# Performance work log

Measured on AMD Instinct MI355X. Metric: run time of the kernel, lower is better.

## Reference

```python
import jax, jax.numpy as jnp
import numpy as np

N_NODES = 50000
N_EDGES = 300000
F_IN, HID, N_CLS = 256, 256, 128


def _glorot_linear(key, fan_in, fan_out):
    # torch.nn.Linear-style uniform init, kaiming bound 1/sqrt(fan_in)
    s = 1.0 / np.sqrt(fan_in)
    return jax.random.uniform(key, (fan_in, fan_out), jnp.float32, -s, s)


def setup_inputs() -> dict:
    key = jax.random.key(0)
    ks = jax.random.split(key, 8)
    x = jax.random.normal(ks[0], (N_NODES, F_IN), jnp.float32)
    edge_index = jax.random.randint(ks[1], (2, N_EDGES), 0, N_NODES, dtype=jnp.int32)
    return {
        "x": x,
        "edge_index": edge_index,
        "W1": _glorot_linear(ks[2], F_IN, HID), "b1": jnp.zeros((HID,), jnp.float32),
        "W2": _glorot_linear(ks[3], HID, HID),  "b2": jnp.zeros((HID,), jnp.float32),
        "W3": _glorot_linear(ks[4], HID, HID),  "b3": jnp.zeros((HID,), jnp.float32),
        "W4": _glorot_linear(ks[5], HID, N_CLS), "b4": jnp.zeros((N_CLS,), jnp.float32),
    }


def _gcn_conv(x, W, b, src, dst, norm, n):
    # x' = D^{-1/2} (A + I) D^{-1/2} X W + b   (PyG GCNConv default)
    h = x @ W                                  # [N, out]
    msg = h[src] * norm[:, None]               # gather + edge scaling  [E', out]
    return jax.ops.segment_sum(msg, dst, num_segments=n) + b


def reference(x, edge_index, W1, b1, W2, b2, W3, b3, W4, b4):
    n = x.shape[0]
    loops = jnp.arange(n, dtype=edge_index.dtype)
    src = jnp.concatenate([edge_index[0], loops])  # add self-loops
    dst = jnp.concatenate([edge_index[1], loops])
    # symmetric normalization: deg over target nodes (unit edge weights)
    deg = jax.ops.segment_sum(jnp.ones_like(dst, jnp.float32), dst, num_segments=n)
    dis = jnp.where(deg > 0, jax.lax.rsqrt(jnp.maximum(deg, 1.0)), 0.0)
    norm = dis[src] * dis[dst]                     # [E']

    h = jax.nn.relu(_gcn_conv(x, W1, b1, src, dst, norm, n))
    h = jax.nn.relu(_gcn_conv(h, W2, b2, src, dst, norm, n))
    h = jax.nn.relu(_gcn_conv(h, W3, b3, src, dst, norm, n))
    h = _gcn_conv(h, W4, b4, src, dst, norm, n)    # [N, C]

    # global_add_pool with batch == zeros -> single-graph sum pool
    pooled = jnp.sum(h, axis=0, keepdims=True)     # [1, C]
    return (pooled, jax.nn.log_softmax(pooled, axis=1))
```

## Files before the change

### kernel.cpp

```cpp
#include <hip/hip_runtime.h>


typedef __attribute__((ext_vector_type(8))) short short8;
typedef __attribute__((ext_vector_type(4))) float float4v;

__device__ __forceinline__ unsigned short f2b(float f) {
    unsigned int u = __builtin_bit_cast(unsigned int, f);
    u += 0x7fffu + ((u >> 16) & 1u);
    return (unsigned short)(u >> 16);
}
__device__ __forceinline__ float b2f(unsigned short b) {
    unsigned int u = ((unsigned int)b) << 16;
    return __builtin_bit_cast(float, u);
}


__global__ void zero_kernel(int* __restrict__ cnt, float* __restrict__ tsum,
                            float* __restrict__ acc, int N) {
    int i = blockIdx.x * 256 + threadIdx.x;
    if (i < N) { cnt[i] = 0; tsum[i] = 0.f; }
    if (i < 256) acc[i] = 0.f;
}

__global__ void count_kernel(const int* __restrict__ dst, int* __restrict__ cnt, int E) {
    int i = blockIdx.x * blockDim.x + threadIdx.x;
    if (i < E) atomicAdd(&cnt[dst[i]], 1);
}

__global__ void blocksum_kernel(const int* __restrict__ cnt, int* __restrict__ bsum, int N) {
    __shared__ int s[256];
    int t = threadIdx.x;
    int i = blockIdx.x * 256 + t;
    s[t] = (i < N) ? cnt[i] : 0;
    __syncthreads();
    for (int d = 128; d > 0; d >>= 1) {
        if (t < d) s[t] += s[t + d];
        __syncthreads();
    }
    if (t == 0) bsum[blockIdx.x] = s[0];
}

__global__ void finalize_kernel(const int* __restrict__ cnt, const int* __restrict__ bsum,
                                int* __restrict__ offs, int* __restrict__ cursor,
                                float* __restrict__ dis, int N, int E, int nb) {
    __shared__ int bs[256];
    __shared__ int s[256];
    int t = threadIdx.x;
    bs[t] = (t < nb) ? bsum[t] : 0;
    __syncthreads();
    for (int d = 1; d < 256; d <<= 1) {
        int x = (t >= d) ? bs[t - d] : 0;
        __syncthreads();
        bs[t] += x;
        __syncthreads();
    }
    int blockoff = (blockIdx.x == 0) ? 0 : bs[blockIdx.x - 1];
    int i = blockIdx.x * 256 + t;
    int c = (i < N) ? cnt[i] : 0;
    s[t] = c;
    __syncthreads();
    for (int d = 1; d < 256; d <<= 1) {
        int x = (t >= d) ? s[t - d] : 0;
        __syncthreads();
        s[t] += x;
        __syncthreads();
    }
    if (i < N) {
        int ex = blockoff + s[t] - c;
        offs[i] = ex;
        cursor[i] = ex;
        dis[i] = rsqrtf((float)(c + 1));
    }
    if (blockIdx.x == 0 && t == 0) offs[N] = E;
}

__global__ void scatter_outsum_kernel(const int* __restrict__ src, const int* __restrict__ dst,
                                      const float* __restrict__ dis, int* __restrict__ cursor,
                                      int* __restrict__ csr_src, float* __restrict__ csr_nrm,
                                      float* __restrict__ tsum, int E) {
    int i = blockIdx.x * blockDim.x + threadIdx.x;
    if (i < E) {
        int s = src[i], d = dst[i];
        float dd = dis[d];
        int pos = atomicAdd(&cursor[d], 1);
        csr_src[pos] = s;
        csr_nrm[pos] = dis[s] * dd;
        atomicAdd(&tsum[s], dd);
    }
}


__global__ void convert_wt_kernel(const float* __restrict__ W1, const float* __restrict__ W2,
                                  const float* __restrict__ W3, unsigned short* __restrict__ Wt1,
                                  unsigned short* __restrict__ Wt2, unsigned short* __restrict__ Wt3) {
    const float* W = (blockIdx.y == 0) ? W1 : (blockIdx.y == 1) ? W2 : W3;
    unsigned short* Wt = (blockIdx.y == 0) ? Wt1 : (blockIdx.y == 1) ? Wt2 : Wt3;
    int n = blockIdx.x;
    int k = threadIdx.x;
    Wt[n * 256 + k] = f2b(W[k * 256 + n]);
}

template <int AFP32>
__global__ __launch_bounds__(256, 3) void gemm_bf16_kernel(
        const void* __restrict__ Ap, const unsigned short* __restrict__ Wt,
        unsigned short* __restrict__ C, int M) {
    __shared__ unsigned short As[128 * 64];
    __shared__ unsigned short Bs[128 * 64];
    const int tid = threadIdx.x;
    const int lane = tid & 63;
    const int wave = tid >> 6;
    const int l15 = lane & 15;
    const int quad = lane >> 4;
    const int wm = wave & 1;
    const int wn = wave >> 1;
    const int m0 = blockIdx.x * 128;
    const int n0 = blockIdx.y * 128;

    float4v acc[4][4] = {};

    const int lrow = lane >> 3;
    const int lslot = (lane & 7) ^ lrow;

    const unsigned short* Bt = Wt + (size_t)n0 * 256;

    for (int kk = 0; kk < 256; kk += 64) {
        if (AFP32) {
            const float* Af = (const float*)Ap;
            const int srow = tid >> 3;
            const int slot = tid & 7;
#pragma unroll
            for (int p = 0; p < 4; p++) {
                int row = p * 32 + srow;
                int gm = m0 + row;
                float4 lo = make_float4(0.f, 0.f, 0.f, 0.f);
                float4 hi = make_float4(0.f, 0.f, 0.f, 0.f);
                if (gm < M) {
                    const float* ap = &Af[(size_t)gm * 256 + kk + slot * 8];
                    lo = *(const float4*)ap;
                    hi = *(const float4*)(ap + 4);
                }
                union { unsigned short u[8]; float4 v; } pk;
                pk.u[0] = f2b(lo.x); pk.u[1] = f2b(lo.y);
                pk.u[2] = f2b(lo.z); pk.u[3] = f2b(lo.w);
                pk.u[4] = f2b(hi.x); pk.u[5] = f2b(hi.y);
                pk.u[6] = f2b(hi.z); pk.u[7] = f2b(hi.w);
                *(float4*)&As[row * 64 + 8 * (slot ^ (row & 7))] = pk.v;
            }
        } else {
            const unsigned short* Ab = (const unsigned short*)Ap;
#pragma unroll
            for (int i = 0; i < 4; i++) {
                int r0 = wave * 32 + i * 8;
                int gm = m0 + r0 + lrow;
                if (gm >= M) gm = M - 1;
                const unsigned short* gp = &Ab[(size_t)gm * 256 + kk + lslot * 8];
                __builtin_amdgcn_global_load_lds(
                    (const __attribute__((address_space(1))) unsigned int*)gp,
                    (__attribute__((address_space(3))) unsigned int*)&As[r0 * 64],
                    16, 0, 0);
            }
        }
#pragma unroll
        for (int i = 0; i < 4; i++) {
            int r0 = wave * 32 + i * 8;
            const unsigned short* gp = &Bt[(size_t)(r0 + lrow) * 256 + kk + lslot * 8];
            __builtin_amdgcn_global_load_lds(
                (const __attribute__((address_space(1))) unsigned int*)gp,
                (__attribute__((address_space(3))) unsigned int*)&Bs[r0 * 64],
                16, 0, 0);
        }
        __syncthreads();
#pragma unroll
        for (int ks = 0; ks < 64; ks += 32) {
            const int sl = (ks >> 3) + quad;
            short8 af[4], bf[4];
#pragma unroll
            for (int mi = 0; mi < 4; mi++) {
                int row = wm * 64 + mi * 16 + l15;
                af[mi] = *(const short8*)&As[row * 64 + 8 * (sl ^ (row & 7))];
            }
#pragma unroll
            for (int nj = 0; nj < 4; nj++) {
                int row = wn * 64 + nj * 16 + l15;
                bf[nj] = *(const short8*)&Bs[row * 64 + 8 * (sl ^ (row & 7))];
            }
#pragma unroll
            for (int mi = 0; mi < 4; mi++)
#pragma unroll
                for (int nj = 0; nj < 4; nj++)
                    acc[mi][nj] = __builtin_amdgcn_mfma_f32_16x16x32_bf16(
                        af[mi], bf[nj], acc[mi][nj], 0, 0, 0);
        }
        __syncthreads();
    }

#pragma unroll
    for (int mi = 0; mi < 4; mi++) {
#pragma unroll
        for (int r = 0; r < 4; r++) {
            int row = m0 + wm * 64 + mi * 16 + quad * 4 + r;
            if (row < M) {
#pragma unroll
                for (int nj = 0; nj < 4; nj++) {
                    int col = n0 + wn * 64 + nj * 16 + l15;
                    C[(size_t)row * 256 + col] = f2b(acc[mi][nj][r]);
                }
            }
        }
    }
}

template <int RELU>
__global__ __launch_bounds__(256) void agg_bf16_kernel(
        const unsigned short* __restrict__ T, const float* __restrict__ bias,
        const int* __restrict__ offs, const int* __restrict__ csr_src,
        const float* __restrict__ csr_nrm, const float* __restrict__ dis,
        unsigned short* __restrict__ out, int N) {
    int hw = threadIdx.x >> 5;
    int l = threadIdx.x & 31;
    int v = blockIdx.x * 8 + hw;
    if (v >= N) return;
    int f8 = l * 8;
    int beg = offs[v], end = offs[v + 1];
    float dv = dis[v];
    float w = dv * dv;
    float a[8];
    {
        short8 hs = *(const short8*)&T[(size_t)v * 256 + f8];
#pragma unroll
        for (int i = 0; i < 8; i++) a[i] = w * b2f((unsigned short)hs[i]);
    }
    int e = beg;
    for (; e + 4 <= end; e += 4) {
        int s0 = csr_src[e],     s1 = csr_src[e + 1];
        int s2 = csr_src[e + 2], s3 = csr_src[e + 3];
        float n0 = csr_nrm[e],     n1 = csr_nrm[e + 1];
        float n2 = csr_nrm[e + 2], n3 = csr_nrm[e + 3];
        short8 h0 = *(const short8*)&T[(size_t)s0 * 256 + f8];
        short8 h1 = *(const short8*)&T[(size_t)s1 * 256 + f8];
        short8 h2 = *(const short8*)&T[(size_t)s2 * 256 + f8];
        short8 h3 = *(const short8*)&T[(size_t)s3 * 256 + f8];
#pragma unroll
        for (int i = 0; i < 8; i++)
            a[i] += n0 * b2f((unsigned short)h0[i]) + n1 * b2f((unsigned short)h1[i])
                  + n2 * b2f((unsigned short)h2[i]) + n3 * b2f((unsigned short)h3[i]);
    }
    for (; e < end; e++) {
        int s = csr_src[e];
        float nm = csr_nrm[e];
        short8 h = *(const short8*)&T[(size_t)s * 256 + f8];
#pragma unroll
        for (int i = 0; i < 8; i++) a[i] += nm * b2f((unsigned short)h[i]);
    }
    float4 bv0 = *(const float4*)&bias[f8];
    float4 bv1 = *(const float4*)&bias[f8 + 4];
    a[0] += bv0.x; a[1] += bv0.y; a[2] += bv0.z; a[3] += bv0.w;
    a[4] += bv1.x; a[5] += bv1.y; a[6] += bv1.z; a[7] += bv1.w;
    if (RELU) {
#pragma unroll
        for (int i = 0; i < 8; i++) a[i] = fmaxf(a[i], 0.f);
    }
    uint4 o;
    o.x = (unsigned int)f2b(a[0]) | ((unsigned int)f2b(a[1]) << 16);
    o.y = (unsigned int)f2b(a[2]) | ((unsigned int)f2b(a[3]) << 16);
    o.z = (unsigned int)f2b(a[4]) | ((unsigned int)f2b(a[5]) << 16);
    o.w = (unsigned int)f2b(a[6]) | ((unsigned int)f2b(a[7]) << 16);
    *(uint4*)&out[(size_t)v * 256 + f8] = o;
}

__global__ __launch_bounds__(256) void wpool_partial(
        const unsigned short* __restrict__ H, const float* __restrict__ dis,
        const float* __restrict__ tsum, float* __restrict__ partial, int N) {
    int tid = threadIdx.x;
    int f8 = (tid & 31) * 8;
    int rg = tid >> 5;
    float a[8] = {};
    for (int r = blockIdx.x * 8 + rg; r < N; r += gridDim.x * 8) {
        float s = dis[r] * (dis[r] + tsum[r]);
        short8 h = *(const short8*)&H[(size_t)r * 256 + f8];
#pragma unroll
        for (int i = 0; i < 8; i++) a[i] += s * b2f((unsigned short)h[i]);
    }
    __shared__ float red[8 * 256];
#pragma unroll
    for (int i = 0; i < 8; i++) red[rg * 256 + f8 + i] = a[i];
    __syncthreads();
    for (int s = 4; s > 0; s >>= 1) {
        if (rg < s) {
#pragma unroll
            for (int i = 0; i < 8; i++)
                red[rg * 256 + f8 + i] += red[(rg + s) * 256 + f8 + i];
        }
        __syncthreads();
    }
    partial[(size_t)blockIdx.x * 256 + tid] = red[tid];
}

__global__ void wpool_reduce(const float* __restrict__ partial, float* __restrict__ acc) {
    int f = threadIdx.x;
    int p0 = blockIdx.x * 32;
    float a = 0.f;
#pragma unroll
    for (int p = 0; p < 32; p++) a += partial[(size_t)(p0 + p) * 256 + f];
    atomicAdd(&acc[f], a);
}

__global__ void final_kernel(const float* __restrict__ acc, const float* __restrict__ W4,
                             const float* __restrict__ b4, float* __restrict__ out, int N) {
    __shared__ float red[128];
    int c = threadIdx.x;
    float p = (float)N * b4[c];
    for (int k = 0; k < 256; k++) p += acc[k] * W4[k * 128 + c];
    out[c] = p;
    red[c] = p;
    __syncthreads();
    for (int s = 64; s > 0; s >>= 1) {
        if (c < s) red[c] = fmaxf(red[c], red[c + s]);
        __syncthreads();
    }
    float m = red[0];
    __syncthreads();
    red[c] = expf(p - m);
    __syncthreads();
    for (int s = 64; s > 0; s >>= 1) {
        if (c < s) red[c] += red[c + s];
        __syncthreads();
    }
    float lse = m + logf(red[0]);
    out[128 + c] = p - lse;
}

extern "C" void kernel_launch(void* const* d_in, const int* in_sizes, int n_in,
                              void* d_out, int out_size, void* d_ws, size_t ws_size,
                              hipStream_t stream) {
    const float* x  = (const float*)d_in[0];
    const int*   ei = (const int*)d_in[1];
    const float* W1 = (const float*)d_in[2];
    const float* b1 = (const float*)d_in[3];
    const float* W2 = (const float*)d_in[4];
    const float* b2 = (const float*)d_in[5];
    const float* W3 = (const float*)d_in[6];
    const float* b3 = (const float*)d_in[7];
    const float* W4 = (const float*)d_in[8];
    const float* b4 = (const float*)d_in[9];

    const int N = in_sizes[0] / 256;
    const int E = in_sizes[1] / 2;
    const int* src = ei;
    const int* dst = ei + E;

    char* p = (char*)d_ws;
    auto alloc = [&](size_t bytes) {
        char* r = p;
        p += (bytes + 255) & ~(size_t)255;
        return r;
    };
    int*            cnt     = (int*)alloc((size_t)N * 4);
    int*            offs    = (int*)alloc((size_t)(N + 1) * 4);
    int*            cursor  = (int*)alloc((size_t)N * 4);
    float*          dis     = (float*)alloc((size_t)N * 4);
    float*          tsum    = (float*)alloc((size_t)N * 4);
    int*            bsum    = (int*)alloc(1024 * 4);
    int*            csr_src = (int*)alloc((size_t)E * 4);
    float*          csr_nrm = (float*)alloc((size_t)E * 4);
    unsigned short* Wt1     = (unsigned short*)alloc(256 * 256 * 2);
    unsigned short* Wt2     = (unsigned short*)alloc(256 * 256 * 2);
    unsigned short* Wt3     = (unsigned short*)alloc(256 * 256 * 2);
    unsigned short* T       = (unsigned short*)alloc((size_t)N * 256 * 2);
    unsigned short* Abuf    = (unsigned short*)alloc((size_t)N * 256 * 2);
    float*          partial = (float*)alloc((size_t)1024 * 256 * 4);
    float*          accbuf  = (float*)alloc(256 * 4);

    int eb = (E + 255) / 256;
    int nb = (N + 255) / 256;
    zero_kernel<<<nb, 256, 0, stream>>>(cnt, tsum, accbuf, N);
    count_kernel<<<eb, 256, 0, stream>>>(dst, cnt, E);
    blocksum_kernel<<<nb, 256, 0, stream>>>(cnt, bsum, N);
    finalize_kernel<<<nb, 256, 0, stream>>>(cnt, bsum, offs, cursor, dis, N, E, nb);
    scatter_outsum_kernel<<<eb, 256, 0, stream>>>(src, dst, dis, cursor, csr_src,
                                                  csr_nrm, tsum, E);

    convert_wt_kernel<<<dim3(256, 3), 256, 0, stream>>>(W1, W2, W3, Wt1, Wt2, Wt3);

    dim3 ggrid((N + 127) / 128, 2);
    int ab = (N + 7) / 8;
    gemm_bf16_kernel<1><<<ggrid, 256, 0, stream>>>(x, Wt1, T, N);
    agg_bf16_kernel<1><<<ab, 256, 0, stream>>>(T, b1, offs, csr_src, csr_nrm, dis, Abuf, N);
    gemm_bf16_kernel<0><<<ggrid, 256, 0, stream>>>(Abuf, Wt2, T, N);
    agg_bf16_kernel<1><<<ab, 256, 0, stream>>>(T, b2, offs, csr_src, csr_nrm, dis, Abuf, N);
    gemm_bf16_kernel<0><<<ggrid, 256, 0, stream>>>(Abuf, Wt3, T, N);
    agg_bf16_kernel<1><<<ab, 256, 0, stream>>>(T, b3, offs, csr_src, csr_nrm, dis, Abuf, N);

    wpool_partial<<<1024, 256, 0, stream>>>(Abuf, dis, tsum, partial, N);
    wpool_reduce<<<32, 256, 0, stream>>>(partial, accbuf);
    final_kernel<<<1, 128, 0, stream>>>(accbuf, W4, b4, (float*)d_out, N);
}
```

Baseline: 312.0 us.

## Degree-sort nodes for aggregation balance and merge small setup kernels

Builds a permutation of nodes bucketed by in-degree (histogram in finalize, counting-sort in a new kernel) so aggregation half-waves in a block process nodes of similar degree, reducing divergence and imbalance. Also fuses the zeroing and weight-conversion kernels into one launch. It drops the separate pool-reduce kernel by having the final kernel sum 256 partials directly. This adds an extra indirection per node, costs locality of output writes, and makes the final kernel do a serial reduction in a single block.

```diff
diff --git a/kernel.cpp b/kernel.cpp
--- a/kernel.cpp
+++ b/kernel.cpp
@@ -14,12 +14,26 @@
     return __builtin_bit_cast(float, u);
 }
 
-
-__global__ void zero_kernel(int* __restrict__ cnt, float* __restrict__ tsum,
-                            float* __restrict__ acc, int N) {
-    int i = blockIdx.x * 256 + threadIdx.x;
-    if (i < N) { cnt[i] = 0; tsum[i] = 0.f; }
-    if (i < 256) acc[i] = 0.f;
+__global__ void zero_convert_kernel(int* __restrict__ cnt, float* __restrict__ tsum,
+                                    int* __restrict__ hist, int* __restrict__ hcur,
+                                    const float* __restrict__ W1, const float* __restrict__ W2,
+                                    const float* __restrict__ W3, unsigned short* __restrict__ Wt1,
+                                    unsigned short* __restrict__ Wt2, unsigned short* __restrict__ Wt3,
+                                    int N, int nb) {
+    int t = threadIdx.x;
+    int b = blockIdx.x;
+    if (b < nb) {
+        int i = b * 256 + t;
+        if (i < N) { cnt[i] = 0; tsum[i] = 0.f; }
+        if (b == 0 && t < 64) { hist[t] = 0; hcur[t] = 0; }
+    } else {
+        int bb = b - nb;
+        int w = bb >> 8;
+        int n = bb & 255;
+        const float* W = (w == 0) ? W1 : (w == 1) ? W2 : W3;
+        unsigned short* Wt = (w == 0) ? Wt1 : (w == 1) ? Wt2 : Wt3;
+        Wt[n * 256 + t] = f2b(W[t * 256 + n]);
+    }
 }
 
 __global__ void count_kernel(const int* __restrict__ dst, int* __restrict__ cnt, int E) {
@@ -42,7 +56,8 @@
 
 __global__ void finalize_kernel(const int* __restrict__ cnt, const int* __restrict__ bsum,
                                 int* __restrict__ offs, int* __restrict__ cursor,
-                                float* __restrict__ dis, int N, int E, int nb) {
+                                float* __restrict__ dis, int* __restrict__ hist,
+                                int N, int E, int nb) {
     __shared__ int bs[256];
     __shared__ int s[256];
     int t = threadIdx.x;
@@ -70,6 +85,7 @@
         offs[i] = ex;
         cursor[i] = ex;
         dis[i] = rsqrtf((float)(c + 1));
+        atomicAdd(&hist[c < 63 ? c : 63], 1);
     }
     if (blockIdx.x == 0 && t == 0) offs[N] = E;
 }
@@ -89,15 +105,32 @@
     }
 }
 
-
-__global__ void convert_wt_kernel(const float* __restrict__ W1, const float* __restrict__ W2,
-                                  const float* __restrict__ W3, unsigned short* __restrict__ Wt1,
-                                  unsigned short* __restrict__ Wt2, unsigned short* __restrict__ Wt3) {
-    const float* W = (blockIdx.y == 0) ? W1 : (blockIdx.y == 1) ? W2 : W3;
-    unsigned short* Wt = (blockIdx.y == 0) ? Wt1 : (blockIdx.y == 1) ? Wt2 : Wt3;
-    int n = blockIdx.x;
-    int k = threadIdx.x;
-    Wt[n * 256 + k] = f2b(W[k * 256 + n]);
+__global__ void permbuild_kernel(const int* __restrict__ cnt, const int* __restrict__ hist,
+                                 int* __restrict__ hcur, int* __restrict__ perm, int N) {
+    __shared__ int s[64];
+    __shared__ int base[64];
+    int t = threadIdx.x;
+    if (t < 64) s[t] = hist[t];
+    __syncthreads();
+    if (t < 64) {
+        for (int d = 1; d < 64; d <<= 1) {
+            int x = (t >= d) ? s[t - d] : 0;
+            __syncthreads();
+            s[t] += x;
+            __syncthreads();
+        }
+        base[t] = s[t] - hist[t];
+    } else {
+        for (int d = 1; d < 64; d <<= 1) { __syncthreads(); __syncthreads(); }
+    }
+    __syncthreads();
+    int i = blockIdx.x * 256 + t;
+    if (i < N) {
+        int c = cnt[i];
+        int b = c < 63 ? c : 63;
+        int pos = base[b] + atomicAdd(&hcur[b], 1);
+        perm[pos] = i;
+    }
 }
 
 template <int AFP32>
@@ -215,11 +248,13 @@
         const unsigned short* __restrict__ T, const float* __restrict__ bias,
         const int* __restrict__ offs, const int* __restrict__ csr_src,
         const float* __restrict__ csr_nrm, const float* __restrict__ dis,
+        const int* __restrict__ perm,
         unsigned short* __restrict__ out, int N) {
     int hw = threadIdx.x >> 5;
     int l = threadIdx.x & 31;
-    int v = blockIdx.x * 8 + hw;
-    if (v >= N) return;
+    int idx = blockIdx.x * 8 + hw;
+    if (idx >= N) return;
+    int v = perm[idx];
     int f8 = l * 8;
     int beg = offs[v], end = offs[v + 1];
     float dv = dis[v];
@@ -296,38 +331,38 @@
     partial[(size_t)blockIdx.x * 256 + tid] = red[tid];
 }
 
-__global__ void wpool_reduce(const float* __restrict__ partial, float* __restrict__ acc) {
-    int f = threadIdx.x;
-    int p0 = blockIdx.x * 32;
-    float a = 0.f;
-#pragma unroll
-    for (int p = 0; p < 32; p++) a += partial[(size_t)(p0 + p) * 256 + f];
-    atomicAdd(&acc[f], a);
-}
-
-__global__ void final_kernel(const float* __restrict__ acc, const float* __restrict__ W4,
+__global__ void final_kernel(const float* __restrict__ partial, const float* __restrict__ W4,
                              const float* __restrict__ b4, float* __restrict__ out, int N) {
+    __shared__ float acc[256];
     __shared__ float red[128];
-    int c = threadIdx.x;
-    float p = (float)N * b4[c];
-    for (int k = 0; k < 256; k++) p += acc[k] * W4[k * 128 + c];
-    out[c] = p;
-    red[c] = p;
+    int t = threadIdx.x;
+    float a0 = 0.f, a1 = 0.f;
+    for (int p = 0; p < 256; p++) {
+        a0 += partial[(size_t)p * 256 + t];
+        a1 += partial[(size_t)p * 256 + t + 128];
+    }
+    acc[t] = a0;
+    acc[t + 128] = a1;
+    __syncthreads();
+    float pv = (float)N * b4[t];
+    for (int k = 0; k < 256; k++) pv += acc[k] * W4[k * 128 + t];
+    out[t] = pv;
+    red[t] = pv;
     __syncthreads();
     for (int s = 64; s > 0; s >>= 1) {
-        if (c < s) red[c] = fmaxf(red[c], red[c + s]);
+        if (t < s) red[t] = fmaxf(red[t], red[t + s]);
         __syncthreads();
     }
     float m = red[0];
     __syncthreads();
-    red[c] = expf(p - m);
+    red[t] = expf(pv - m);
     __syncthreads();
     for (int s = 64; s > 0; s >>= 1) {
-        if (c < s) red[c] += red[c + s];
+        if (t < s) red[t] += red[t + s];
         __syncthreads();
     }
     float lse = m + logf(red[0]);
-    out[128 + c] = p - lse;
+    out[128 + t] = pv - lse;
 }
 
 extern "C" void kernel_launch(void* const* d_in, const int* in_sizes, int n_in,
@@ -361,6 +396,9 @@
     float*          dis     = (float*)alloc((size_t)N * 4);
     float*          tsum    = (float*)alloc((size_t)N * 4);
     int*            bsum    = (int*)alloc(1024 * 4);
+    int*            hist    = (int*)alloc(64 * 4);
+    int*            hcur    = (int*)alloc(64 * 4);
+    int*            perm    = (int*)alloc((size_t)N * 4);
     int*            csr_src = (int*)alloc((size_t)E * 4);
     float*          csr_nrm = (float*)alloc((size_t)E * 4);
     unsigned short* Wt1     = (unsigned short*)alloc(256 * 256 * 2);
@@ -368,30 +406,28 @@
     unsigned short* Wt3     = (unsigned short*)alloc(256 * 256 * 2);
     unsigned short* T       = (unsigned short*)alloc((size_t)N * 256 * 2);
     unsigned short* Abuf    = (unsigned short*)alloc((size_t)N * 256 * 2);
-    float*          partial = (float*)alloc((size_t)1024 * 256 * 4);
-    float*          accbuf  = (float*)alloc(256 * 4);
+    float*          partial = (float*)alloc((size_t)256 * 256 * 4);
 
     int eb = (E + 255) / 256;
     int nb = (N + 255) / 256;
-    zero_kernel<<<nb, 256, 0, stream>>>(cnt, tsum, accbuf, N);
+    zero_convert_kernel<<<nb + 768, 256, 0, stream>>>(cnt, tsum, hist, hcur,
+                                                      W1, W2, W3, Wt1, Wt2, Wt3, N, nb);
     count_kernel<<<eb, 256, 0, stream>>>(dst, cnt, E);
     blocksum_kernel<<<nb, 256, 0, stream>>>(cnt, bsum, N);
-    finalize_kernel<<<nb, 256, 0, stream>>>(cnt, bsum, offs, cursor, dis, N, E, nb);
+    finalize_kernel<<<nb, 256, 0, stream>>>(cnt, bsum, offs, cursor, dis, hist, N, E, nb);
     scatter_outsum_kernel<<<eb, 256, 0, stream>>>(src, dst, dis, cursor, csr_src,
                                                   csr_nrm, tsum, E);
-
-    convert_wt_kernel<<<dim3(256, 3), 256, 0, stream>>>(W1, W2, W3, Wt1, Wt2, Wt3);
+    permbuild_kernel<<<nb, 256, 0, stream>>>(cnt, hist, hcur, perm, N);
 
     dim3 ggrid((N + 127) / 128, 2);
     int ab = (N + 7) / 8;
     gemm_bf16_kernel<1><<<ggrid, 256, 0, stream>>>(x, Wt1, T, N);
-    agg_bf16_kernel<1><<<ab, 256, 0, stream>>>(T, b1, offs, csr_src, csr_nrm, dis, Abuf, N);
+    agg_bf16_kernel<1><<<ab, 256, 0, stream>>>(T, b1, offs, csr_src, csr_nrm, dis, perm, Abuf, N);
     gemm_bf16_kernel<0><<<ggrid, 256, 0, stream>>>(Abuf, Wt2, T, N);
-    agg_bf16_kernel<1><<<ab, 256, 0, stream>>>(T, b2, offs, csr_src, csr_nrm, dis, Abuf, N);
+    agg_bf16_kernel<1><<<ab, 256, 0, stream>>>(T, b2, offs, csr_src, csr_nrm, dis, perm, Abuf, N);
     gemm_bf16_kernel<0><<<ggrid, 256, 0, stream>>>(Abuf, Wt3, T, N);
-    agg_bf16_kernel<1><<<ab, 256, 0, stream>>>(T, b3, offs, csr_src, csr_nrm, dis, Abuf, N);
-
-    wpool_partial<<<1024, 256, 0, stream>>>(Abuf, dis, tsum, partial, N);
-    wpool_reduce<<<32, 256, 0, stream>>>(partial, accbuf);
-    final_kernel<<<1, 128, 0, stream>>>(accbuf, W4, b4, (float*)d_out, N);
-}
+    agg_bf16_kernel<1><<<ab, 256, 0, stream>>>(T, b3, offs, csr_src, csr_nrm, dis, perm, Abuf, N);
+
+    wpool_partial<<<256, 256, 0, stream>>>(Abuf, dis, tsum, partial, N);
+    final_kernel<<<1, 128, 0, stream>>>(partial, W4, b4, (float*)d_out, N);
+}
```

Result: slower. 699.9 us (+124.3%).

## Quantize GEMM output to int8 with per-row-half scales for aggregation gathers

Applied to the files above, without the earlier changes.

The GEMM epilogue now computes a per-row absmax over each 128-column half, writes an fp32 scale and int8-quantized values instead of bf16. The aggregation kernel gathers int8 neighbor rows and folds the per-source scale into the edge norm, halving the bytes moved by the random gathers. The zero-init and weight-conversion kernels are also merged into one launch. Int8 quantization of intermediate features lowers precision and may push the result outside the tolerance, and each edge now needs an extra scale load.

```diff
diff --git a/kernel.cpp b/kernel.cpp
--- a/kernel.cpp
+++ b/kernel.cpp
@@ -2,6 +2,7 @@
 
 
 typedef __attribute__((ext_vector_type(8))) short short8;
+typedef __attribute__((ext_vector_type(8))) signed char schar8;
 typedef __attribute__((ext_vector_type(4))) float float4v;
 
 __device__ __forceinline__ unsigned short f2b(float f) {
@@ -14,12 +15,26 @@
     return __builtin_bit_cast(float, u);
 }
 
-
-__global__ void zero_kernel(int* __restrict__ cnt, float* __restrict__ tsum,
-                            float* __restrict__ acc, int N) {
-    int i = blockIdx.x * 256 + threadIdx.x;
-    if (i < N) { cnt[i] = 0; tsum[i] = 0.f; }
-    if (i < 256) acc[i] = 0.f;
+__global__ void zero_convert_kernel(int* __restrict__ cnt, float* __restrict__ tsum,
+                                    float* __restrict__ accbuf,
+                                    const float* __restrict__ W1, const float* __restrict__ W2,
+                                    const float* __restrict__ W3, unsigned short* __restrict__ Wt1,
+                                    unsigned short* __restrict__ Wt2, unsigned short* __restrict__ Wt3,
+                                    int N, int nb) {
+    int t = threadIdx.x;
+    int b = blockIdx.x;
+    if (b < nb) {
+        int i = b * 256 + t;
+        if (i < N) { cnt[i] = 0; tsum[i] = 0.f; }
+        if (b == 0) accbuf[t] = 0.f;
+    } else {
+        int bb = b - nb;
+        int w = bb >> 8;
+        int n = bb & 255;
+        const float* W = (w == 0) ? W1 : (w == 1) ? W2 : W3;
+        unsigned short* Wt = (w == 0) ? Wt1 : (w == 1) ? Wt2 : Wt3;
+        Wt[n * 256 + t] = f2b(W[t * 256 + n]);
+    }
 }
 
 __global__ void count_kernel(const int* __restrict__ dst, int* __restrict__ cnt, int E) {
@@ -89,21 +104,10 @@
     }
 }
 
-
-__global__ void convert_wt_kernel(const float* __restrict__ W1, const float* __restrict__ W2,
-                                  const float* __restrict__ W3, unsigned short* __restrict__ Wt1,
-                                  unsigned short* __restrict__ Wt2, unsigned short* __restrict__ Wt3) {
-    const float* W = (blockIdx.y == 0) ? W1 : (blockIdx.y == 1) ? W2 : W3;
-    unsigned short* Wt = (blockIdx.y == 0) ? Wt1 : (blockIdx.y == 1) ? Wt2 : Wt3;
-    int n = blockIdx.x;
-    int k = threadIdx.x;
-    Wt[n * 256 + k] = f2b(W[k * 256 + n]);
-}
-
 template <int AFP32>
 __global__ __launch_bounds__(256, 3) void gemm_bf16_kernel(
         const void* __restrict__ Ap, const unsigned short* __restrict__ Wt,
-        unsigned short* __restrict__ C, int M) {
+        signed char* __restrict__ C8, float* __restrict__ Ts, int M) {
     __shared__ unsigned short As[128 * 64];
     __shared__ unsigned short Bs[128 * 64];
     const int tid = threadIdx.x;
@@ -194,16 +198,44 @@
         __syncthreads();
     }
 
+    float* pmax = (float*)As;
+    float* pinv = (float*)Bs;
 #pragma unroll
     for (int mi = 0; mi < 4; mi++) {
 #pragma unroll
         for (int r = 0; r < 4; r++) {
-            int row = m0 + wm * 64 + mi * 16 + quad * 4 + r;
+            float m = fabsf(acc[mi][0][r]);
+            m = fmaxf(m, fabsf(acc[mi][1][r]));
+            m = fmaxf(m, fabsf(acc[mi][2][r]));
+            m = fmaxf(m, fabsf(acc[mi][3][r]));
+            m = fmaxf(m, __shfl_xor(m, 1));
+            m = fmaxf(m, __shfl_xor(m, 2));
+            m = fmaxf(m, __shfl_xor(m, 4));
+            m = fmaxf(m, __shfl_xor(m, 8));
+            if (l15 == 0) pmax[(wm * 64 + mi * 16 + quad * 4 + r) * 2 + wn] = m;
+        }
+    }
+    __syncthreads();
+    if (tid < 128) {
+        float m = fmaxf(pmax[tid * 2], pmax[tid * 2 + 1]);
+        int grow = m0 + tid;
+        if (grow < M) Ts[(size_t)grow * 2 + blockIdx.y] = m * (1.f / 127.f);
+        pinv[tid] = (m > 0.f) ? 127.f / m : 0.f;
+    }
+    __syncthreads();
+#pragma unroll
+    for (int mi = 0; mi < 4; mi++) {
+#pragma unroll
+        for (int r = 0; r < 4; r++) {
+            int lr = wm * 64 + mi * 16 + quad * 4 + r;
+            float inv = pinv[lr];
+            int row = m0 + lr;
             if (row < M) {
 #pragma unroll
                 for (int nj = 0; nj < 4; nj++) {
                     int col = n0 + wn * 64 + nj * 16 + l15;
-                    C[(size_t)row * 256 + col] = f2b(acc[mi][nj][r]);
+                    C8[(size_t)row * 256 + col] =
+                        (signed char)__float2int_rn(acc[mi][nj][r] * inv);
                 }
             }
         }
@@ -212,7 +244,8 @@
 
 template <int RELU>
 __global__ __launch_bounds__(256) void agg_bf16_kernel(
-        const unsigned short* __restrict__ T, const float* __restrict__ bias,
+        const signed char* __restrict__ T8, const float* __restrict__ Ts,
+        const float* __restrict__ bias,
         const int* __restrict__ offs, const int* __restrict__ csr_src,
         const float* __restrict__ csr_nrm, const float* __restrict__ dis,
         unsigned short* __restrict__ out, int N) {
@@ -221,36 +254,39 @@
     int v = blockIdx.x * 8 + hw;
     if (v >= N) return;
     int f8 = l * 8;
+    int hh = l >> 4;
     int beg = offs[v], end = offs[v + 1];
     float dv = dis[v];
-    float w = dv * dv;
+    float w = dv * dv * Ts[(size_t)v * 2 + hh];
     float a[8];
     {
-        short8 hs = *(const short8*)&T[(size_t)v * 256 + f8];
-#pragma unroll
-        for (int i = 0; i < 8; i++) a[i] = w * b2f((unsigned short)hs[i]);
+        schar8 q = *(const schar8*)&T8[(size_t)v * 256 + f8];
+#pragma unroll
+        for (int i = 0; i < 8; i++) a[i] = w * (float)q[i];
     }
     int e = beg;
     for (; e + 4 <= end; e += 4) {
         int s0 = csr_src[e],     s1 = csr_src[e + 1];
         int s2 = csr_src[e + 2], s3 = csr_src[e + 3];
-        float n0 = csr_nrm[e],     n1 = csr_nrm[e + 1];
-        float n2 = csr_nrm[e + 2], n3 = csr_nrm[e + 3];
-        short8 h0 = *(const short8*)&T[(size_t)s0 * 256 + f8];
-        short8 h1 = *(const short8*)&T[(size_t)s1 * 256 + f8];
-        short8 h2 = *(const short8*)&T[(size_t)s2 * 256 + f8];
-        short8 h3 = *(const short8*)&T[(size_t)s3 * 256 + f8];
+        float n0 = csr_nrm[e]     * Ts[(size_t)s0 * 2 + hh];
+        float n1 = csr_nrm[e + 1] * Ts[(size_t)s1 * 2 + hh];
+        float n2 = csr_nrm[e + 2] * Ts[(size_t)s2 * 2 + hh];
+        float n3 = csr_nrm[e + 3] * Ts[(size_t)s3 * 2 + hh];
+        schar8 h0 = *(const schar8*)&T8[(size_t)s0 * 256 + f8];
+        schar8 h1 = *(const schar8*)&T8[(size_t)s1 * 256 + f8];
+        schar8 h2 = *(const schar8*)&T8[(size_t)s2 * 256 + f8];
+        schar8 h3 = *(const schar8*)&T8[(size_t)s3 * 256 + f8];
 #pragma unroll
         for (int i = 0; i < 8; i++)
-            a[i] += n0 * b2f((unsigned short)h0[i]) + n1 * b2f((unsigned short)h1[i])
-                  + n2 * b2f((unsigned short)h2[i]) + n3 * b2f((unsigned short)h3[i]);
+            a[i] += n0 * (float)h0[i] + n1 * (float)h1[i]
+                  + n2 * (float)h2[i] + n3 * (float)h3[i];
     }
     for (; e < end; e++) {
         int s = csr_src[e];
-        float nm = csr_nrm[e];
-        short8 h = *(const short8*)&T[(size_t)s * 256 + f8];
-#pragma unroll
-        for (int i = 0; i < 8; i++) a[i] += nm * b2f((unsigned short)h[i]);
+        float nm = csr_nrm[e] * Ts[(size_t)s * 2 + hh];
+        schar8 h = *(const schar8*)&T8[(size_t)s * 256 + f8];
+#pragma unroll
+        for (int i = 0; i < 8; i++) a[i] += nm * (float)h[i];
     }
     float4 bv0 = *(const float4*)&bias[f8];
     float4 bv1 = *(const float4*)&bias[f8 + 4];
@@ -366,30 +402,30 @@
     unsigned short* Wt1     = (unsigned short*)alloc(256 * 256 * 2);
     unsigned short* Wt2     = (unsigned short*)alloc(256 * 256 * 2);
     unsigned short* Wt3     = (unsigned short*)alloc(256 * 256 * 2);
-    unsigned short* T       = (unsigned short*)alloc((size_t)N * 256 * 2);
+    signed char*    T8      = (signed char*)alloc((size_t)N * 256);
+    float*          Ts      = (float*)alloc((size_t)N * 2 * 4);
     unsigned short* Abuf    = (unsigned short*)alloc((size_t)N * 256 * 2);
     float*          partial = (float*)alloc((size_t)1024 * 256 * 4);
     float*          accbuf  = (float*)alloc(256 * 4);
 
     int eb = (E + 255) / 256;
     int nb = (N + 255) / 256;
-    zero_kernel<<<nb, 256, 0, stream>>>(cnt, tsum, accbuf, N);
+    zero_convert_kernel<<<nb + 768, 256, 0, stream>>>(cnt, tsum, accbuf,
+                                                      W1, W2, W3, Wt1, Wt2, Wt3, N, nb);
     count_kernel<<<eb, 256, 0, stream>>>(dst, cnt, E);
     blocksum_kernel<<<nb, 256, 0, stream>>>(cnt, bsum, N);
     finalize_kernel<<<nb, 256, 0, stream>>>(cnt, bsum, offs, cursor, dis, N, E, nb);
     scatter_outsum_kernel<<<eb, 256, 0, stream>>>(src, dst, dis, cursor, csr_src,
                                                   csr_nrm, tsum, E);
 
-    convert_wt_kernel<<<dim3(256, 3), 256, 0, stream>>>(W1, W2, W3, Wt1, Wt2, Wt3);
-
     dim3 ggrid((N + 127) / 128, 2);
     int ab = (N + 7) / 8;
-    gemm_bf16_kernel<1><<<ggrid, 256, 0, stream>>>(x, Wt1, T, N);
-    agg_bf16_kernel<1><<<ab, 256, 0, stream>>>(T, b1, offs, csr_src, csr_nrm, dis, Abuf, N);
-    gemm_bf16_kernel<0><<<ggrid, 256, 0, stream>>>(Abuf, Wt2, T, N);
-    agg_bf16_kernel<1><<<ab, 256, 0, stream>>>(T, b2, offs, csr_src, csr_nrm, dis, Abuf, N);
-    gemm_bf16_kernel<0><<<ggrid, 256, 0, stream>>>(Abuf, Wt3, T, N);
-    agg_bf16_kernel<1><<<ab, 256, 0, stream>>>(T, b3, offs, csr_src, csr_nrm, dis, Abuf, N);
+    gemm_bf16_kernel<1><<<ggrid, 256, 0, stream>>>(x, Wt1, T8, Ts, N);
+    agg_bf16_kernel<1><<<ab, 256, 0, stream>>>(T8, Ts, b1, offs, csr_src, csr_nrm, dis, Abuf, N);
+    gemm_bf16_kernel<0><<<ggrid, 256, 0, stream>>>(Abuf, Wt2, T8, Ts, N);
+    agg_bf16_kernel<1><<<ab, 256, 0, stream>>>(T8, Ts, b2, offs, csr_src, csr_nrm, dis, Abuf, N);
+    gemm_bf16_kernel<0><<<ggrid, 256, 0, stream>>>(Abuf, Wt3, T8, Ts, N);
+    agg_bf16_kernel<1><<<ab, 256, 0, stream>>>(T8, Ts, b3, offs, csr_src, csr_nrm, dis, Abuf, N);
 
     wpool_partial<<<1024, 256, 0, stream>>>(Abuf, dis, tsum, partial, N);
     wpool_reduce<<<32, 256, 0, stream>>>(partial, accbuf);
```

After: 314.1 us. About the same (+0.7%).
